# Optimization experiments

Measured on AMD Instinct MI355X. Metric: run time of the kernel, lower is better.

The kernel has to match this reference:

```python
import jax, jax.numpy as jnp
import numpy as np

OUT_H, OUT_W = 7, 7
SPATIAL_SCALE = 1.0


def setup_inputs() -> dict:
    key = jax.random.key(0)
    B, C, H, W = 4, 256, 64, 64
    N = 128
    features = jax.random.normal(key, (B, C, H, W), dtype=jnp.float32)
    rng = np.random.default_rng(0)
    bidx = rng.integers(0, B, N)
    x1 = rng.integers(0, W - 8, N)
    y1 = rng.integers(0, H - 8, N)
    x2 = np.minimum(x1 + rng.integers(4, 48, N), W - 1)
    y2 = np.minimum(y1 + rng.integers(4, 48, N), H - 1)
    rois = jnp.asarray(np.stack([bidx, x1, y1, x2, y2], axis=1), dtype=jnp.int32)
    return {"features": features, "rois": rois}


def _bin_bounds(n_bins, bin_sz, roi_sz):
    # h_start = int(h*bin_h); h_end = int((h+1)*bin_h); then clamp as in torch code
    bins = jnp.arange(n_bins)
    start = jnp.floor(bins[None, :] * bin_sz[:, None]).astype(jnp.int32)
    end = jnp.floor((bins[None, :] + 1) * bin_sz[:, None]).astype(jnp.int32)
    start = jnp.minimum(start, roi_sz[:, None] - 1)
    end = jnp.minimum(end, roi_sz[:, None])
    return start, end  # [N, n_bins]


def _roi_pool(features, rois):
    B, C, H, W = features.shape
    b = rois[:, 0]
    coords = (rois[:, 1:5].astype(jnp.float32) * SPATIAL_SCALE).astype(jnp.int32)
    x1, y1, x2, y2 = coords[:, 0], coords[:, 1], coords[:, 2], coords[:, 3]
    roi_h = y2 - y1 + 1  # inclusive slice y1:y2+1
    roi_w = x2 - x1 + 1
    bin_h = roi_h.astype(jnp.float32) / OUT_H
    bin_w = roi_w.astype(jnp.float32) / OUT_W

    hs, he = _bin_bounds(OUT_H, bin_h, roi_h)  # [N, OUT_H]
    ws, we = _bin_bounds(OUT_W, bin_w, roi_w)  # [N, OUT_W]
    valid = (he > hs)[:, :, None] & (we > ws)[:, None, :]  # [N, OUT_H, OUT_W]

    yy = jnp.arange(H)
    xx = jnp.arange(W)
    # absolute-coordinate bin masks (factorized along H and W)
    mask_h = (yy[None, None, :] >= (y1[:, None] + hs)[:, :, None]) & (
        yy[None, None, :] < (y1[:, None] + he)[:, :, None])  # [N, OUT_H, H]
    mask_w = (xx[None, None, :] >= (x1[:, None] + ws)[:, :, None]) & (
        xx[None, None, :] < (x1[:, None] + we)[:, :, None])  # [N, OUT_W, W]

    feat = features[b]  # [N, C, H, W] gather per ROI
    NEG = jnp.array(-jnp.inf, features.dtype)
    # reduce H per output row bin (OUT_H is small, fixed)
    rows = [jnp.where(mask_h[:, i, None, :, None], feat, NEG).max(axis=2)
            for i in range(OUT_H)]  # each [N, C, W]
    rowmax = jnp.stack(rows, axis=1)  # [N, OUT_H, C, W]
    cols = [jnp.where(mask_w[:, j, None, None, :], rowmax, NEG).max(axis=3)
            for j in range(OUT_W)]  # each [N, OUT_H, C]
    pooled = jnp.stack(cols, axis=3)  # [N, OUT_H, C, OUT_W]
    pooled = jnp.transpose(pooled, (0, 2, 1, 3))  # [N, C, OUT_H, OUT_W]
    # empty bins (h_end<=h_start or w_end<=w_start) stay zero, as in the torch code
    return jnp.where(valid[:, None, :, :], pooled, jnp.zeros((), features.dtype))


def reference(features, rois):
    return _roi_pool(features, rois)
```

## Files before the change

### kernel.cpp

```cpp
#include <hip/hip_runtime.h>
#include <math.h>

#define OUT_H 7
#define OUT_W 7

__global__ __launch_bounds__(256) void roipool_kernel(
    const float* __restrict__ feat, const int* __restrict__ rois,
    float* __restrict__ out, int total, int C, int H, int W)
{
    int idx = blockIdx.x * blockDim.x + threadIdx.x;
    if (idx >= total) return;

    int pw = idx % OUT_W;
    int t  = idx / OUT_W;
    int ph = t % OUT_H;
    t /= OUT_H;
    int c = t % 256;
    int n = t / 256;

    const int* r = rois + n * 5;
    int b  = r[0];
    int x1 = r[1];
    int y1 = r[2];
    int x2 = r[3];
    int y2 = r[4];

    int roi_h = y2 - y1 + 1;
    int roi_w = x2 - x1 + 1;

    int hs = (ph * roi_h) / OUT_H;
    int he = ((ph + 1) * roi_h) / OUT_H;
    hs = hs < (roi_h - 1) ? hs : (roi_h - 1);
    he = he < roi_h ? he : roi_h;

    int ws = (pw * roi_w) / OUT_W;
    int we = ((pw + 1) * roi_w) / OUT_W;
    ws = ws < (roi_w - 1) ? ws : (roi_w - 1);
    we = we < roi_w ? we : roi_w;

    float result = 0.0f;
    if (he > hs && we > ws) {
        float m = -INFINITY;
        const float* base =
            feat + (((size_t)b * (size_t)C + (size_t)c) * (size_t)H) * (size_t)W;
        for (int y = y1 + hs; y < y1 + he; ++y) {
            const float* row = base + (size_t)y * (size_t)W + (size_t)x1;
            for (int x = ws; x < we; ++x) {
                m = fmaxf(m, row[x]);
            }
        }
        result = m;
    }
    out[idx] = result;
}

extern "C" void kernel_launch(void* const* d_in, const int* in_sizes, int n_in,
                              void* d_out, int out_size, void* d_ws, size_t ws_size,
                              hipStream_t stream) {
    const float* feat = (const float*)d_in[0];
    const int*   rois = (const int*)d_in[1];
    float*       out  = (float*)d_out;

    const int C = 256, H = 64, W = 64;
    const int N = in_sizes[1] / 5;
    const int total = N * C * OUT_H * OUT_W;

    int block = 256;
    int grid = (total + block - 1) / block;
    roipool_kernel<<<grid, block, 0, stream>>>(feat, rois, out, total, C, H, W);
}
```

Baseline: 84.12 us.

## Transpose features to channels-last and pool with one channel per thread

Adds a tiled shared-memory transpose kernel that rewrites features from NCHW to NHWC in the workspace. The pooling kernel then assigns one block per ROI bin and one thread per channel, so each pixel read is coalesced across the block instead of strided per thread. This costs an extra full pass over the 16 MB feature tensor plus a second kernel launch. Output writes become strided by the bin count.

New measurement: 96.66 us. 14.9% more time.

```diff
diff --git a/kernel.cpp b/kernel.cpp
--- a/kernel.cpp
+++ b/kernel.cpp
@@ -3,30 +3,67 @@
 
 #define OUT_H 7
 #define OUT_W 7
+#define NBINS (OUT_H * OUT_W)
 
-__global__ __launch_bounds__(256) void roipool_kernel(
-    const float* __restrict__ feat, const int* __restrict__ rois,
-    float* __restrict__ out, int total, int C, int H, int W)
+__global__ __launch_bounds__(256) void transpose_kernel(
+    const float* __restrict__ in, float* __restrict__ out, int C, int P)
 {
-    int idx = blockIdx.x * blockDim.x + threadIdx.x;
-    if (idx >= total) return;
+    __shared__ float tile[64][65];
 
-    int pw = idx % OUT_W;
-    int t  = idx / OUT_W;
-    int ph = t % OUT_H;
-    t /= OUT_H;
-    int c = t % 256;
-    int n = t / 256;
+    const int pt = blockIdx.x;
+    const int ct = blockIdx.y;
+    const int b  = blockIdx.z;
+
+    const int p0 = pt * 64;
+    const int c0 = ct * 64;
+
+    const int pq = threadIdx.x & 15;
+    const int cr = threadIdx.x >> 4;
+
+    #pragma unroll
+    for (int k = 0; k < 4; ++k) {
+        int c_local = cr + 16 * k;
+        const float4 v = *(const float4*)&in[((size_t)(b * C + c0 + c_local)) * P + p0 + pq * 4];
+        tile[c_local][pq * 4 + 0] = v.x;
+        tile[c_local][pq * 4 + 1] = v.y;
+        tile[c_local][pq * 4 + 2] = v.z;
+        tile[c_local][pq * 4 + 3] = v.w;
+    }
+    __syncthreads();
+
+    #pragma unroll
+    for (int k = 0; k < 4; ++k) {
+        int p_local = cr + 16 * k;
+        float4 w;
+        w.x = tile[pq * 4 + 0][p_local];
+        w.y = tile[pq * 4 + 1][p_local];
+        w.z = tile[pq * 4 + 2][p_local];
+        w.w = tile[pq * 4 + 3][p_local];
+        *(float4*)&out[((size_t)(b * P + p0 + p_local)) * C + c0 + pq * 4] = w;
+    }
+}
+
+__global__ __launch_bounds__(256) void pool_kernel(
+    const float* __restrict__ featT,
+    const int* __restrict__ rois,
+    float* __restrict__ out, int C, int H, int W)
+{
+    const int bin = blockIdx.x % NBINS;
+    const int n   = blockIdx.x / NBINS;
+    const int c   = threadIdx.x;
+
+    const int ph = bin / OUT_W;
+    const int pw = bin % OUT_W;
 
     const int* r = rois + n * 5;
-    int b  = r[0];
-    int x1 = r[1];
-    int y1 = r[2];
-    int x2 = r[3];
-    int y2 = r[4];
+    const int b  = r[0];
+    const int x1 = r[1];
+    const int y1 = r[2];
+    const int x2 = r[3];
+    const int y2 = r[4];
 
-    int roi_h = y2 - y1 + 1;
-    int roi_w = x2 - x1 + 1;
+    const int roi_h = y2 - y1 + 1;
+    const int roi_w = x2 - x1 + 1;
 
     int hs = (ph * roi_h) / OUT_H;
     int he = ((ph + 1) * roi_h) / OUT_H;
@@ -41,17 +78,18 @@
     float result = 0.0f;
     if (he > hs && we > ws) {
         float m = -INFINITY;
-        const float* base =
-            feat + (((size_t)b * (size_t)C + (size_t)c) * (size_t)H) * (size_t)W;
-        for (int y = y1 + hs; y < y1 + he; ++y) {
-            const float* row = base + (size_t)y * (size_t)W + (size_t)x1;
-            for (int x = ws; x < we; ++x) {
-                m = fmaxf(m, row[x]);
+        const int y_lo = y1 + hs, y_hi = y1 + he;
+        const int x_lo = x1 + ws, x_hi = x1 + we;
+        for (int y = y_lo; y < y_hi; ++y) {
+            const float* rowp = featT + (((size_t)b * (H * W) + (size_t)y * W + x_lo) * C) + c;
+            for (int x = x_lo; x < x_hi; ++x) {
+                m = fmaxf(m, *rowp);
+                rowp += C;
             }
         }
         result = m;
     }
-    out[idx] = result;
+    out[((size_t)(n * C + c)) * NBINS + bin] = result;
 }
 
 extern "C" void kernel_launch(void* const* d_in, const int* in_sizes, int n_in,
@@ -60,12 +98,15 @@
     const float* feat = (const float*)d_in[0];
     const int*   rois = (const int*)d_in[1];
     float*       out  = (float*)d_out;
+    float*       featT = (float*)d_ws;
 
     const int C = 256, H = 64, W = 64;
+    const int P = H * W;
+    const int B = 4;
     const int N = in_sizes[1] / 5;
-    const int total = N * C * OUT_H * OUT_W;
 
-    int block = 256;
-    int grid = (total + block - 1) / block;
-    roipool_kernel<<<grid, block, 0, stream>>>(feat, rois, out, total, C, H, W);
+    dim3 tgrid(P / 64, C / 64, B);
+    transpose_kernel<<<tgrid, 256, 0, stream>>>(feat, featT, C, P);
+
+    pool_kernel<<<N * NBINS, 256, 0, stream>>>(featT, rois, out, C, H, W);
 }
```

## Restructure ROI pooling into per-wave row-max reduction with LDS column pass

Applied to the files above, without the earlier changes.

Each block now handles one ROI and four channels, with one wave per channel. Each lane reads one full-width column and takes a max over the rows of each output-row bin, giving coalesced 64-wide loads. Lanes then reduce columns from LDS into bins. This replaces the old thread-per-output-bin scheme, which did scattered, uncoalesced reads. The cost is block-wide syncs per bin row, and most threads sit idle during the column pass.

After: 98.30 us. +16.9%, slower.

```diff
diff --git a/kernel.cpp b/kernel.cpp
--- a/kernel.cpp
+++ b/kernel.cpp
@@ -3,55 +3,77 @@
 
 #define OUT_H 7
 #define OUT_W 7
+#define NBINS 49
+#define CPB 4
 
-__global__ __launch_bounds__(256) void roipool_kernel(
+__global__ __launch_bounds__(256) void roipool_fused(
     const float* __restrict__ feat, const int* __restrict__ rois,
-    float* __restrict__ out, int total, int C, int H, int W)
+    float* __restrict__ out)
 {
-    int idx = blockIdx.x * blockDim.x + threadIdx.x;
-    if (idx >= total) return;
+    constexpr int C = 256, H = 64, W = 64;
+    __shared__ float racc_lds[CPB * 64];
+    __shared__ float pooled[CPB * NBINS];
 
-    int pw = idx % OUT_W;
-    int t  = idx / OUT_W;
-    int ph = t % OUT_H;
-    t /= OUT_H;
-    int c = t % 256;
-    int n = t / 256;
+    const int bx = blockIdx.x;
+    const int n  = bx >> 6;
+    const int c0 = (bx & 63) * CPB;
+
+    const int tid  = threadIdx.x;
+    const int lane = tid & 63;
+    const int wave = tid >> 6;
+    const int c    = c0 + wave;
+
+    if (tid < CPB * NBINS) pooled[tid] = 0.0f;
 
     const int* r = rois + n * 5;
-    int b  = r[0];
-    int x1 = r[1];
-    int y1 = r[2];
-    int x2 = r[3];
-    int y2 = r[4];
+    const int b  = r[0];
+    const int x1 = r[1];
+    const int y1 = r[2];
+    const int x2 = r[3];
+    const int y2 = r[4];
+    const int roi_h = y2 - y1 + 1;
+    const int roi_w = x2 - x1 + 1;
 
-    int roi_h = y2 - y1 + 1;
-    int roi_w = x2 - x1 + 1;
+    const float* plane = feat + ((size_t)(b * C + c)) * (H * W);
 
-    int hs = (ph * roi_h) / OUT_H;
-    int he = ((ph + 1) * roi_h) / OUT_H;
-    hs = hs < (roi_h - 1) ? hs : (roi_h - 1);
-    he = he < roi_h ? he : roi_h;
+    __syncthreads();
 
-    int ws = (pw * roi_w) / OUT_W;
-    int we = ((pw + 1) * roi_w) / OUT_W;
-    ws = ws < (roi_w - 1) ? ws : (roi_w - 1);
-    we = we < roi_w ? we : roi_w;
+    for (int ph = 0; ph < OUT_H; ++ph) {
+        int hs = (ph * roi_h) / OUT_H;
+        int he = ((ph + 1) * roi_h) / OUT_H;
+        hs = hs < roi_h - 1 ? hs : roi_h - 1;
+        he = he < roi_h ? he : roi_h;
+        const bool ph_valid = (he > hs);
 
-    float result = 0.0f;
-    if (he > hs && we > ws) {
-        float m = -INFINITY;
-        const float* base =
-            feat + (((size_t)b * (size_t)C + (size_t)c) * (size_t)H) * (size_t)W;
-        for (int y = y1 + hs; y < y1 + he; ++y) {
-            const float* row = base + (size_t)y * (size_t)W + (size_t)x1;
-            for (int x = ws; x < we; ++x) {
-                m = fmaxf(m, row[x]);
+        if (ph_valid) {
+            float racc = -INFINITY;
+            for (int y = y1 + hs; y < y1 + he; ++y) {
+                racc = fmaxf(racc, plane[y * W + lane]);
+            }
+            racc_lds[wave * 64 + lane] = racc;
+        }
+        __syncthreads();
+
+        if (ph_valid && tid < CPB * OUT_W) {
+            const int pw = tid % OUT_W;
+            const int cw = tid / OUT_W;
+            int ws = (pw * roi_w) / OUT_W;
+            int we = ((pw + 1) * roi_w) / OUT_W;
+            ws = ws < roi_w - 1 ? ws : roi_w - 1;
+            we = we < roi_w ? we : roi_w;
+            if (we > ws) {
+                float m = -INFINITY;
+                const float* seg = &racc_lds[cw * 64 + x1];
+                for (int x = ws; x < we; ++x) m = fmaxf(m, seg[x]);
+                pooled[cw * NBINS + ph * OUT_W + pw] = m;
             }
         }
-        result = m;
+        __syncthreads();
     }
-    out[idx] = result;
+
+    if (tid < CPB * NBINS) {
+        out[((size_t)(n * C + c0)) * NBINS + tid] = pooled[tid];
+    }
 }
 
 extern "C" void kernel_launch(void* const* d_in, const int* in_sizes, int n_in,
@@ -61,11 +83,8 @@
     const int*   rois = (const int*)d_in[1];
     float*       out  = (float*)d_out;
 
-    const int C = 256, H = 64, W = 64;
     const int N = in_sizes[1] / 5;
-    const int total = N * C * OUT_H * OUT_W;
+    const int n_blocks = N * (256 / CPB);
 
-    int block = 256;
-    int grid = (total + block - 1) / block;
-    roipool_kernel<<<grid, block, 0, stream>>>(feat, rois, out, total, C, H, W);
+    roipool_fused<<<n_blocks, 256, 0, stream>>>(feat, rois, out);
 }
```
